# Optimization experiments

Hardware: AMD Instinct MI355X
Metric: run time of the kernel (lower is better)

Reference implementation:

```python
import jax, jax.numpy as jnp
import numpy as np

B, CIN, H, W = 2, 55, 768, 768
NR, NC = 24, 24      # number of grid-cell rows / cols
CTOP = 36            # block_conv1x1_output[block_num-1] for block_num=2


def _dil_conv_relu(x, w, b, dil):
    # Conv2d(k=5, dilation=dil, padding=2*dil) -> same spatial size, then ReLU
    pad = 2 * dil
    y = jax.lax.conv_general_dilated(
        x, w, window_strides=(1, 1), padding=[(pad, pad), (pad, pad)],
        rhs_dilation=(dil, dil), dimension_numbers=('NCHW', 'OIHW', 'NCHW'))
    return jax.nn.relu(y + b[None, :, None, None])


def setup_inputs() -> dict:
    key = jax.random.key(0)
    ks = jax.random.split(key, 12)
    def p(k, shape, fan_in):
        bound = 1.0 / np.sqrt(fan_in)
        return jax.random.uniform(k, shape, jnp.float32, -bound, bound)
    return {
        'x': jax.random.normal(ks[0], (B, CIN, H, W), dtype=jnp.float32),
        'row_ids': jnp.sort(jax.random.randint(ks[1], (H,), 0, NR)).astype(jnp.int32),
        'col_ids': jnp.sort(jax.random.randint(ks[2], (W,), 0, NC)).astype(jnp.int32),
        'num_row_segs': NR,
        'num_col_segs': NC,
        'w1': p(ks[3], (6, CIN, 5, 5), CIN * 25), 'b1': p(ks[4], (6,), CIN * 25),
        'w2': p(ks[5], (6, CIN, 5, 5), CIN * 25), 'b2': p(ks[6], (6,), CIN * 25),
        'w3': p(ks[7], (6, CIN, 5, 5), CIN * 25), 'b3': p(ks[8], (6,), CIN * 25),
        'w_top': p(ks[9], (CTOP, 18), 18), 'b_top': p(ks[9], (CTOP,), 18),
        'w_bot': p(ks[10], (1, 18), 18), 'b_bot': p(ks[11], (1,), 18),
    }


def reference(x, row_ids, col_ids, num_row_segs, num_col_segs,
              w1, b1, w2, b2, w3, b3, w_top, b_top, w_bot, b_bot):
    b = x.shape[0]
    # --- three dilated conv branches, concat on channels ---
    x1 = _dil_conv_relu(x, w1, b1, 1)
    x2 = _dil_conv_relu(x, w2, b2, 2)
    x3 = _dil_conv_relu(x, w3, b3, 3)
    out_feature = jnp.concatenate((x1, x2, x3), axis=1)  # [B,18,H,W]

    # 1x1 convs as channel matmuls
    top = jnp.einsum('oi,bihw->bohw', w_top, out_feature) + b_top[None, :, None, None]
    bot = jnp.einsum('oi,bihw->bohw', w_bot, out_feature) + b_bot[None, :, None, None]

    # segment one-hot selectors: R [NR,H], C [NC,W]
    R = (row_ids[None, :] == jnp.arange(num_row_segs, dtype=row_ids.dtype)[:, None]).astype(x.dtype)
    C = (col_ids[None, :] == jnp.arange(num_col_segs, dtype=col_ids.dtype)[:, None]).astype(x.dtype)
    cnt = jnp.maximum(R.sum(1)[:, None] * C.sum(1)[None, :], 1.0)  # [NR,NC] cell sizes

    # --- top branch: per-(batch,channel) grid-cell mean, broadcast back ---
    top_sums = jnp.einsum('rh,bkhw,cw->bkrc', R, top, C)           # [B,CTOP,NR,NC]
    top_means = top_sums / cnt
    top_out = top_means[:, :, row_ids, :][:, :, :, col_ids]        # [B,CTOP,H,W]

    # --- bottom branch: mean of sigmoid over cell AND batch (torch.mean over all dims) ---
    sig = jax.nn.sigmoid(bot)                                      # [B,1,H,W]
    bot_sums = jnp.einsum('rh,bkhw,cw->rc', R, sig, C)             # [NR,NC]
    pools_val = bot_sums / (b * cnt)
    bottom_out = jnp.broadcast_to(pools_val[row_ids, :][:, col_ids][None, None],
                                  (b, 1, top.shape[2], top.shape[3]))
    pools = jnp.broadcast_to(pools_val[None, None], (b, 1, num_row_segs, num_col_segs))

    out_x = jnp.concatenate((top_out, out_feature, bottom_out), axis=1)  # [B,55,H,W]
    return out_x, pools
```

## Files before the change

### kernel.cpp

```cpp
#include <hip/hip_runtime.h>
#include <math.h>

#define HH 768
#define WW 768
#define NPIX (HH*WW)
#define NRR 24
#define NCC 24
#define NCELL (NRR*NCC)
#define CTOPC 36
#define NB 2

typedef _Float16 f16x8 __attribute__((ext_vector_type(8)));
typedef float f32x4 __attribute__((ext_vector_type(4)));

__device__ __forceinline__ size_t xt_off(int b) {
  return b ? (size_t)54 * NPIX : 0;
}

#define OFF_WB     0
#define OFF_ZP     38400
#define OFF_FSUM   38656
#define OFF_BOTP   59392
#define OFF_TMEAN  60544
#define OFF_PVAL   102016
#define OFF_BOUNDS 102592

__global__ void prep_kernel(const float* __restrict__ w1, const float* __restrict__ w2,
                            const float* __restrict__ w3,
                            const int* __restrict__ row_ids, const int* __restrict__ col_ids,
                            unsigned int* __restrict__ wB, unsigned int* __restrict__ zp,
                            int* __restrict__ bounds) {
  int t = blockIdx.x * 256 + threadIdx.x;
  if (t < 150 * 256) {
    int frag = t >> 8, r = t & 255;
    int lane = r >> 2, part = r & 3;
    int chb = frag & 1, q = frag >> 1;
    int d = q / 25, tap = q % 25;
    int ky = tap / 5, kx = tap % 5;
    int oc = lane & 15;
    int kk = (lane >> 4) * 8 + part * 2;
    int ch0 = chb * 32 + kk, ch1 = ch0 + 1;
    const float* ws_ = (d == 0) ? w1 : ((d == 1) ? w2 : w3);
    float f0 = (oc < 6 && ch0 < 55) ? ws_[((oc * 55 + ch0) * 5 + ky) * 5 + kx] : 0.f;
    float f1 = (oc < 6 && ch1 < 55) ? ws_[((oc * 55 + ch1) * 5 + ky) * 5 + kx] : 0.f;
    _Float16 g0 = (_Float16)f0, g1 = (_Float16)f1;
    wB[t] = (unsigned int)__builtin_bit_cast(unsigned short, g0) |
            ((unsigned int)__builtin_bit_cast(unsigned short, g1) << 16);
  }
  if (blockIdx.x == 1 && threadIdx.x < 256) zp[threadIdx.x] = 0u;
  if (blockIdx.x == 0 && threadIdx.x < 48) {
    int tt = threadIdx.x;
    const int* ids = (tt < 24) ? row_ids : col_ids;
    int r = tt % 24;
    int s = HH, e = HH;
    for (int h = 0; h < HH; ++h) {
      int v = ids[h];
      if (v >= r && h < s) s = h;
      if (v >= r + 1 && h < e) e = h;
    }
    int base = (tt < 24) ? 0 : 48;
    bounds[base + r] = s;
    bounds[base + 24 + r] = e;
  }
}

__global__ __launch_bounds__(256) void xpose_kernel(const float* __restrict__ x,
                                                    unsigned int* __restrict__ outU) {
  const int b = blockIdx.y;
  const int px = blockIdx.x * 256 + threadIdx.x;
  const float* xb = x + (size_t)b * 55 * NPIX + px;
  unsigned int buf[32];
  #pragma unroll
  for (int cp = 0; cp < 27; ++cp) {
    float f0 = xb[(size_t)(2 * cp) * NPIX];
    float f1 = xb[(size_t)(2 * cp + 1) * NPIX];
    buf[cp] = __builtin_bit_cast(unsigned int, __builtin_amdgcn_cvt_pkrtz(f0, f1));
  }
  buf[27] = __builtin_bit_cast(unsigned int, __builtin_amdgcn_cvt_pkrtz(xb[(size_t)54 * NPIX], 0.f));
  buf[28] = buf[29] = buf[30] = buf[31] = 0u;
  unsigned int* dst = outU + xt_off(b) + (size_t)px * 32;
  #pragma unroll
  for (int i = 0; i < 8; ++i) ((uint4*)dst)[i] = *(uint4*)&buf[i * 4];
}

__global__ __attribute__((amdgpu_flat_work_group_size(384, 384)))
           __attribute__((amdgpu_waves_per_eu(2, 3)))
void conv_kernel(const unsigned int* __restrict__ outU_c,
                 const unsigned int* __restrict__ wB,
                 const unsigned int* __restrict__ zp,
                 const float* __restrict__ b1, const float* __restrict__ b2,
                 const float* __restrict__ b3, float* __restrict__ out) {
  __shared__ __align__(16) unsigned int tile[14080];
  const int tid = threadIdx.x;
  const int lane = tid & 63, wave = tid >> 6;
  const int d = wave >> 1, hh = wave & 1, dil = d + 1;
  const int b = blockIdx.z;
  const int h0 = blockIdx.y * 8, w0 = blockIdx.x * 32;
  const unsigned int* xTb = outU_c + xt_off(b);
  const int col = lane & 15, kq = lane >> 4;

  f32x4 acc[8];
  #pragma unroll
  for (int u = 0; u < 8; ++u) acc[u] = (f32x4){0.f, 0.f, 0.f, 0.f};

  for (int chb = 0; chb < 2; ++chb) {
    #pragma unroll
    for (int k = 0; k < 10; ++k) {
      int i = k * 384 + tid;
      if (i < 3520) {
        int pxl = i % 880, q = i / 880;
        int th = pxl / 44, tw = pxl % 44;
        int gh = h0 - 6 + th, gw = w0 - 6 + tw;
        bool ok = ((unsigned)gh < 768u) & ((unsigned)gw < 768u);
        uint4 v = make_uint4(0u, 0u, 0u, 0u);
        if (ok) v = *(const uint4*)(xTb + ((size_t)(gh * 768 + gw)) * 32 + chb * 16 + q * 4);
        int slot = q ^ ((pxl >> 1) & 3);
        *(uint4*)&tile[pxl * 16 + slot * 4] = v;
      }
    }
    __syncthreads();
    for (int ky = 0; ky < 5; ++ky) {
      #pragma unroll
      for (int kx = 0; kx < 5; ++kx) {
        const int fidx = ((d * 25 + ky * 5 + kx) * 2 + chb) << 8;
        f16x8 bfrag = __builtin_bit_cast(f16x8, *(const uint4*)(wB + fidx + lane * 4));
        const int dy = (ky - 2) * dil, dx = (kx - 2) * dil;
        const int thb = hh * 4 + 6 + dy;
        const int twb = col + 6 + dx;
        #pragma unroll
        for (int u = 0; u < 8; ++u) {
          int hr = u >> 1, pc = u & 1;
          int pxl = (thb + hr) * 44 + twb + pc * 16;
          int slot = kq ^ ((pxl >> 1) & 3);
          f16x8 afrag = __builtin_bit_cast(f16x8, *(const uint4*)&tile[pxl * 16 + slot * 4]);
          acc[u] = __builtin_amdgcn_mfma_f32_16x16x32_f16(afrag, bfrag, acc[u], 0, 0, 0);
        }
      }
    }
    __syncthreads();
  }

  float* ot = (float*)tile;
  if (col < 6) {
    #pragma unroll
    for (int u = 0; u < 8; ++u) {
      int hr = hh * 4 + (u >> 1), pc = u & 1;
      int oc = d * 6 + col;
      #pragma unroll
      for (int reg = 0; reg < 4; ++reg) {
        int px = kq * 4 + reg;
        ot[(oc * 8 + hr) * 32 + pc * 16 + px] = acc[u][reg];
      }
    }
  }
  __syncthreads();
  #pragma unroll
  for (int k = 0; k < 3; ++k) {
    int i = k * 384 + tid;
    int oc = i >> 6, rem = i & 63;
    int hr = rem >> 3, f4 = rem & 7;
    float bias = oc < 6 ? b1[oc] : (oc < 12 ? b2[oc - 6] : b3[oc - 12]);
    float4 v = ((float4*)ot)[i];
    v.x = fmaxf(v.x + bias, 0.f); v.y = fmaxf(v.y + bias, 0.f);
    v.z = fmaxf(v.z + bias, 0.f); v.w = fmaxf(v.w + bias, 0.f);
    *(float4*)(out + ((size_t)(b * 55 + 36 + oc)) * NPIX
               + (size_t)(h0 + hr) * 768 + w0 + f4 * 4) = v;
  }
}

__global__ __launch_bounds__(256) void cellsum_kernel(const float* __restrict__ dout,
    const int* __restrict__ bounds,
    const float* __restrict__ w_bot, const float* __restrict__ b_bot,
    float* __restrict__ feat_sums, float* __restrict__ bot_partial) {
  int blk = blockIdx.x;
  int b = blk / NCELL; int rc = blk % NCELL; int r = rc / NCC, c = rc % NCC;
  int rs = bounds[r], re = bounds[24 + r], cs = bounds[48 + c], ce = bounds[72 + c];
  int cw = ce - cs;
  int npix = (re - rs) * cw;
  float facc[18];
  #pragma unroll
  for (int k = 0; k < 18; ++k) facc[k] = 0.f;
  float sacc = 0.f;
  float wb[18];
  #pragma unroll
  for (int k = 0; k < 18; ++k) wb[k] = w_bot[k];
  float bb = b_bot[0];
  const float* fb = dout + ((size_t)b * 55 + 36) * NPIX;
  for (int i = threadIdx.x; i < npix; i += 256) {
    int hh = rs + i / cw, ww = cs + i % cw;
    int pix = hh * WW + ww;
    float dot = bb;
    #pragma unroll
    for (int k = 0; k < 18; ++k) {
      float v = fb[(size_t)k * NPIX + pix];
      facc[k] += v;
      dot += wb[k] * v;
    }
    sacc += 1.f / (1.f + expf(-dot));
  }
  #pragma unroll
  for (int k = 0; k < 18; ++k) {
    #pragma unroll
    for (int off = 32; off; off >>= 1) facc[k] += __shfl_xor(facc[k], off);
  }
  #pragma unroll
  for (int off = 32; off; off >>= 1) sacc += __shfl_xor(sacc, off);
  __shared__ float red[4][19];
  int wv = threadIdx.x >> 6, ln = threadIdx.x & 63;
  if (ln == 0) {
    #pragma unroll
    for (int k = 0; k < 18; ++k) red[wv][k] = facc[k];
    red[wv][18] = sacc;
  }
  __syncthreads();
  if (threadIdx.x < 19) {
    float s = red[0][threadIdx.x] + red[1][threadIdx.x] + red[2][threadIdx.x] + red[3][threadIdx.x];
    if (threadIdx.x < 18) feat_sums[(size_t)blk * 18 + threadIdx.x] = s;
    else bot_partial[blk] = s;
  }
}

__global__ void cellmean_kernel(const float* __restrict__ feat_sums,
    const float* __restrict__ bot_partial, const int* __restrict__ bounds,
    const float* __restrict__ w_top, const float* __restrict__ b_top,
    float* __restrict__ top_means, float* __restrict__ pools_val, float* __restrict__ dout) {
  int t = blockIdx.x * 256 + threadIdx.x;
  if (t < NB * CTOPC * NCELL) {
    int c = t % NCC, r = (t / NCC) % NRR, k = (t / NCELL) % CTOPC, b = t / (NCELL * CTOPC);
    int cnt = (bounds[24 + r] - bounds[r]) * (bounds[72 + c] - bounds[48 + c]);
    float v = 0.f;
    if (cnt > 0) {
      const float* fs = feat_sums + ((size_t)(b * NCELL + r * NCC + c)) * 18;
      float dot = 0.f;
      #pragma unroll
      for (int i = 0; i < 18; ++i) dot += w_top[k * 18 + i] * fs[i];
      v = dot / (float)cnt + b_top[k];
    }
    top_means[t] = v;
  }
  int t2 = t - NB * CTOPC * NCELL;
  if (t2 >= 0 && t2 < NCELL) {
    int r = t2 / NCC, c = t2 % NCC;
    int cnt = (bounds[24 + r] - bounds[r]) * (bounds[72 + c] - bounds[48 + c]);
    if (cnt < 1) cnt = 1;
    float v = (bot_partial[t2] + bot_partial[NCELL + t2]) / (2.f * (float)cnt);
    pools_val[t2] = v;
    dout[(size_t)NB * 55 * NPIX + t2] = v;
    dout[(size_t)NB * 55 * NPIX + NCELL + t2] = v;
  }
}

__global__ __launch_bounds__(256) void bcast_kernel(const float* __restrict__ top_means,
    const float* __restrict__ pools_val, const int* __restrict__ row_ids,
    const int* __restrict__ col_ids, float* __restrict__ out) {
  int w = blockIdx.x * 256 + threadIdx.x;
  int h = blockIdx.y;
  int b = blockIdx.z;
  int r = row_ids[h], c = col_ids[w];
  int pix = h * 768 + w;
  float* ob = out + (size_t)b * 55 * NPIX + pix;
  const float* tm = top_means + (size_t)b * CTOPC * NCELL + r * NCC + c;
  #pragma unroll
  for (int k = 0; k < 36; ++k) ob[(size_t)k * NPIX] = tm[(size_t)k * NCELL];
  ob[(size_t)54 * NPIX] = pools_val[r * NCC + c];
}

extern "C" void kernel_launch(void* const* d_in, const int* in_sizes, int n_in,
                              void* d_out, int out_size, void* d_ws, size_t ws_size,
                              hipStream_t stream) {
  const float* x      = (const float*)d_in[0];
  const int* row_ids  = (const int*)d_in[1];
  const int* col_ids  = (const int*)d_in[2];
  const float* w1     = (const float*)d_in[5];
  const float* b1     = (const float*)d_in[6];
  const float* w2     = (const float*)d_in[7];
  const float* b2     = (const float*)d_in[8];
  const float* w3     = (const float*)d_in[9];
  const float* b3     = (const float*)d_in[10];
  const float* w_top  = (const float*)d_in[11];
  const float* b_top  = (const float*)d_in[12];
  const float* w_bot  = (const float*)d_in[13];
  const float* b_bot  = (const float*)d_in[14];
  float* out = (float*)d_out;
  float* ws  = (float*)d_ws;

  unsigned int* wB   = (unsigned int*)ws + OFF_WB;
  unsigned int* zp   = (unsigned int*)ws + OFF_ZP;
  float* feat_sums   = ws + OFF_FSUM;
  float* bot_partial = ws + OFF_BOTP;
  float* top_means   = ws + OFF_TMEAN;
  float* pools_val   = ws + OFF_PVAL;
  int*   bounds      = (int*)ws + OFF_BOUNDS;
  unsigned int* outU = (unsigned int*)d_out;

  hipLaunchKernelGGL(prep_kernel, dim3(150), dim3(256), 0, stream,
                     w1, w2, w3, row_ids, col_ids, wB, zp, bounds);
  hipLaunchKernelGGL(xpose_kernel, dim3(2304, 2), dim3(256), 0, stream,
                     x, outU);
  hipLaunchKernelGGL(conv_kernel, dim3(24, 96, 2), dim3(384), 0, stream,
                     outU, wB, zp, b1, b2, b3, out);
  hipLaunchKernelGGL(cellsum_kernel, dim3(NB * NCELL), dim3(256), 0, stream,
                     out, bounds, w_bot, b_bot, feat_sums, bot_partial);
  hipLaunchKernelGGL(cellmean_kernel, dim3(165), dim3(256), 0, stream,
                     feat_sums, bot_partial, bounds, w_top, b_top, top_means, pools_val, out);
  hipLaunchKernelGGL(bcast_kernel, dim3(3, 768, 2), dim3(256), 0, stream,
                     top_means, pools_val, row_ids, col_ids, out);
}
```

Baseline: 458.0 us.

## Prefetch second channel block into registers during first block's MFMA compute

The conv kernel now issues the global loads for the second 16-channel block into registers before computing on the first block, then writes them to LDS afterwards. This hides global-load latency behind the MFMA work. It also fully unrolls the 25 taps with a one-ahead weight-fragment prefetch and raises wave priority around the MFMA bursts. The cost is about 40 extra VGPRs for staging, which may lower occupancy.

```diff
diff --git a/kernel.cpp b/kernel.cpp
--- a/kernel.cpp
+++ b/kernel.cpp
@@ -103,42 +103,68 @@
   #pragma unroll
   for (int u = 0; u < 8; ++u) acc[u] = (f32x4){0.f, 0.f, 0.f, 0.f};
 
-  for (int chb = 0; chb < 2; ++chb) {
+  uint4 st[10];
+  auto LOADG = [&](int chb) {
     #pragma unroll
     for (int k = 0; k < 10; ++k) {
       int i = k * 384 + tid;
+      st[k] = make_uint4(0u, 0u, 0u, 0u);
       if (i < 3520) {
         int pxl = i % 880, q = i / 880;
         int th = pxl / 44, tw = pxl % 44;
         int gh = h0 - 6 + th, gw = w0 - 6 + tw;
         bool ok = ((unsigned)gh < 768u) & ((unsigned)gw < 768u);
-        uint4 v = make_uint4(0u, 0u, 0u, 0u);
-        if (ok) v = *(const uint4*)(xTb + ((size_t)(gh * 768 + gw)) * 32 + chb * 16 + q * 4);
+        if (ok) st[k] = *(const uint4*)(xTb + ((size_t)(gh * 768 + gw)) * 32 + chb * 16 + q * 4);
+      }
+    }
+  };
+  auto WRITES = [&]() {
+    #pragma unroll
+    for (int k = 0; k < 10; ++k) {
+      int i = k * 384 + tid;
+      if (i < 3520) {
+        int pxl = i % 880, q = i / 880;
         int slot = q ^ ((pxl >> 1) & 3);
-        *(uint4*)&tile[pxl * 16 + slot * 4] = v;
+        *(uint4*)&tile[pxl * 16 + slot * 4] = st[k];
       }
     }
-    __syncthreads();
-    for (int ky = 0; ky < 5; ++ky) {
+  };
+  auto COMPUTE = [&](int chb) {
+    const unsigned int* wBc = wB + (size_t)(d * 25 * 2 + chb) * 256;
+    uint4 bf = *(const uint4*)(wBc + lane * 4);
+    #pragma unroll
+    for (int tap = 0; tap < 25; ++tap) {
+      uint4 bfn = bf;
+      if (tap < 24) bfn = *(const uint4*)(wBc + (size_t)(tap + 1) * 512 + lane * 4);
+      const int ky = tap / 5, kx = tap % 5;
+      const int dy = (ky - 2) * dil, dx = (kx - 2) * dil;
+      const int thb = hh * 4 + 6 + dy;
+      const int twb = col + 6 + dx;
+      f16x8 bfrag = __builtin_bit_cast(f16x8, bf);
+      __builtin_amdgcn_s_setprio(1);
       #pragma unroll
-      for (int kx = 0; kx < 5; ++kx) {
-        const int fidx = ((d * 25 + ky * 5 + kx) * 2 + chb) << 8;
-        f16x8 bfrag = __builtin_bit_cast(f16x8, *(const uint4*)(wB + fidx + lane * 4));
-        const int dy = (ky - 2) * dil, dx = (kx - 2) * dil;
-        const int thb = hh * 4 + 6 + dy;
-        const int twb = col + 6 + dx;
-        #pragma unroll
-        for (int u = 0; u < 8; ++u) {
-          int hr = u >> 1, pc = u & 1;
-          int pxl = (thb + hr) * 44 + twb + pc * 16;
-          int slot = kq ^ ((pxl >> 1) & 3);
-          f16x8 afrag = __builtin_bit_cast(f16x8, *(const uint4*)&tile[pxl * 16 + slot * 4]);
-          acc[u] = __builtin_amdgcn_mfma_f32_16x16x32_f16(afrag, bfrag, acc[u], 0, 0, 0);
-        }
+      for (int u = 0; u < 8; ++u) {
+        int hr = u >> 1, pc = u & 1;
+        int pxl = (thb + hr) * 44 + twb + pc * 16;
+        int slot = kq ^ ((pxl >> 1) & 3);
+        f16x8 afrag = __builtin_bit_cast(f16x8, *(const uint4*)&tile[pxl * 16 + slot * 4]);
+        acc[u] = __builtin_amdgcn_mfma_f32_16x16x32_f16(afrag, bfrag, acc[u], 0, 0, 0);
       }
-    }
-    __syncthreads();
-  }
+      __builtin_amdgcn_s_setprio(0);
+      bf = bfn;
+    }
+  };
+
+  LOADG(0);
+  WRITES();
+  __syncthreads();
+  LOADG(1);
+  COMPUTE(0);
+  __syncthreads();
+  WRITES();
+  __syncthreads();
+  COMPUTE(1);
+  __syncthreads();
 
   float* ot = (float*)tile;
   if (col < 6) {
```

After: 616.1 us. 34.5% more time.
